# Kernel tuning notes

Measured on AMD Instinct MI355X. Metric: run time of the kernel, lower is better.

Reference implementation:

```python
import jax, jax.numpy as jnp
import numpy as np

SEQ, DM, STATE, BATCH = 1024, 512, 16, 8
D2 = 2 * DM
EPS = 1e-5


def rmsnorm(x, w):
    return x * jax.lax.rsqrt(jnp.mean(x * x, axis=-1, keepdims=True) + EPS) * w


def setup_inputs() -> dict:
    key = jax.random.key(0)
    ks = jax.random.split(key, 16)
    def lin(k, i, o):
        k1, k2 = jax.random.split(k)
        s = 1.0 / np.sqrt(i)
        return (jax.random.uniform(k1, (i, o), minval=-s, maxval=s),
                jax.random.uniform(k2, (o,), minval=-s, maxval=s))
    inp_w, inp_b = lin(ks[0], DM, D2)
    convlin_w, convlin_b = lin(ks[1], D2, D2)
    fc1_w, fc1_b = lin(ks[2], D2, D2)
    fc2_w, fc2_b = lin(ks[3], D2, STATE)
    fc3_w, fc3_b = lin(ks[4], D2, STATE)
    D_w, D_b = lin(ks[5], DM, D2)
    out_w, _ = lin(ks[6], D2, DM)
    out_b = jnp.ones((DM,))  # nn.init.constant_(out_proj.bias, 1.0)
    # Conv1d(seq_len, seq_len, k=3): weight (out_ch=SEQ, in_ch=SEQ, 3)
    s = 1.0 / np.sqrt(SEQ * 3)
    conv_w = jax.random.uniform(ks[7], (SEQ, SEQ, 3), minval=-s, maxval=s)
    conv_b = jax.random.uniform(ks[8], (SEQ,), minval=-s, maxval=s)
    norm_w = jnp.ones((DM,))
    x = jax.random.normal(ks[9], (BATCH, SEQ, DM))
    return dict(x=x, norm_w=norm_w, inp_w=inp_w, inp_b=inp_b, conv_w=conv_w,
                conv_b=conv_b, convlin_w=convlin_w, convlin_b=convlin_b,
                fc1_w=fc1_w, fc1_b=fc1_b, fc2_w=fc2_w, fc2_b=fc2_b,
                fc3_w=fc3_w, fc3_b=fc3_b, D_w=D_w, D_b=D_b,
                out_w=out_w, out_b=out_b)


def reference(x, norm_w, inp_w, inp_b, conv_w, conv_b, convlin_w, convlin_b,
              fc1_w, fc1_b, fc2_w, fc2_b, fc3_w, fc3_b, D_w, D_b, out_w, out_b):
    xn = rmsnorm(x, norm_w)                                  # (b, L, d)
    x_proj = xn @ inp_w + inp_b                              # (b, L, 2d)
    # Conv1d over channels=seq_len, spatial=2d, padding=1
    x_conv = jax.lax.conv_general_dilated(
        x_proj, conv_w, window_strides=(1,), padding=[(1, 1)],
        dimension_numbers=('NCH', 'OIH', 'NCH')) + conv_b[None, :, None]
    x_conv_out = jax.nn.silu(x_conv) @ convlin_w + convlin_b  # (b, L, 2d)
    # S6: h starts at zero so dA term vanishes; y = x*delta*sum_n(B*C)
    u = x_conv_out
    B = u @ fc2_w + fc2_b                                     # (b, L, n)
    C = u @ fc3_w + fc3_b                                     # (b, L, n)
    delta = jax.nn.softplus(u @ fc1_w + fc1_b)                # (b, L, 2d)
    bc = jnp.sum(B * C, axis=-1, keepdims=True)               # (b, L, 1)
    x_ssm = u * delta * bc                                    # (b, L, 2d)
    x_act = jax.nn.silu(x_ssm)
    x_residual = jax.nn.silu(xn @ D_w + D_b)
    return (x_residual * x_act) @ out_w + out_b               # (b, L, d)
```

## Files before the change

kernel.cpp:

```cpp
#include <hip/hip_runtime.h>
#include <hip/hip_bf16.h>

#define SEQ 1024
#define DM 512
#define D2 1024
#define NSTATE 16
#define BATCH 8
#define ROWS (BATCH * SEQ)
#define EPSF 1e-5f

typedef __attribute__((ext_vector_type(8))) short bf16x8;
typedef __attribute__((ext_vector_type(4))) float f32x4;

#define AS1 __attribute__((address_space(1)))
#define AS3 __attribute__((address_space(3)))

__device__ __forceinline__ void gll16(const void* g, void* l) {
    __builtin_amdgcn_global_load_lds(
        (const AS1 unsigned int*)(uintptr_t)g,
        (AS3 unsigned int*)(unsigned int)(uintptr_t)l, 16, 0, 0);
}

__device__ __forceinline__ float sigmoidf_(float x) {
    return 1.f / (1.f + __expf(-x));
}
__device__ __forceinline__ unsigned short f2bf(float f) {
    __hip_bfloat16 h = __float2bfloat16(f);
    unsigned short r;
    __builtin_memcpy(&r, &h, 2);
    return r;
}

__global__ __launch_bounds__(256) void tcvt_k(const float* __restrict__ src,
                                              __hip_bfloat16* __restrict__ dst,
                                              int R, int C) {
    __shared__ float tile[32][33];
    int c0 = blockIdx.x * 32, r0 = blockIdx.y * 32;
    int tx = threadIdx.x & 31, ty = threadIdx.x >> 5;
#pragma unroll
    for (int p = 0; p < 4; ++p) {
        int r = r0 + ty + p * 8, c = c0 + tx;
        if (r < R && c < C) tile[ty + p * 8][tx] = src[(size_t)r * C + c];
    }
    __syncthreads();
#pragma unroll
    for (int p = 0; p < 4; ++p) {
        int c = c0 + ty + p * 8, r = r0 + tx;
        if (r < R && c < C)
            dst[(size_t)c * R + r] = __float2bfloat16(tile[tx][ty + p * 8]);
    }
}

__global__ __launch_bounds__(256) void convw_k(const float* __restrict__ cw,
                                               __hip_bfloat16* __restrict__ wk) {
    int idx = blockIdx.x * 256 + threadIdx.x;
    float a = cw[(size_t)idx * 3 + 0];
    float b = cw[(size_t)idx * 3 + 1];
    float c = cw[(size_t)idx * 3 + 2];
    wk[idx] = __float2bfloat16(a);
    wk[(size_t)SEQ * SEQ + idx] = __float2bfloat16(b);
    wk[(size_t)2 * SEQ * SEQ + idx] = __float2bfloat16(c);
}

__global__ __launch_bounds__(256) void rmsnorm_k(
    const float* __restrict__ x, const float* __restrict__ w,
    __hip_bfloat16* __restrict__ o) {
    int row = blockIdx.x;
    const float* xr = x + (size_t)row * DM;
    __hip_bfloat16* orow = o + (size_t)row * DM;
    int t = threadIdx.x;
    float v0 = xr[t];
    float v1 = xr[t + 256];
    float ss = v0 * v0 + v1 * v1;
#pragma unroll
    for (int off = 32; off; off >>= 1) ss += __shfl_down(ss, off, 64);
    __shared__ float parts[4];
    if ((t & 63) == 0) parts[t >> 6] = ss;
    __syncthreads();
    float tot = parts[0] + parts[1] + parts[2] + parts[3];
    float rs = rsqrtf(tot * (1.f / DM) + EPSF);
    orow[t] = __float2bfloat16(v0 * rs * w[t]);
    orow[t + 256] = __float2bfloat16(v1 * rs * w[t + 256]);
}

template <int EPI>
__global__ __launch_bounds__(256) void mgemm(
    const __hip_bfloat16* __restrict__ A, const __hip_bfloat16* __restrict__ Bt,
    const float* __restrict__ bias, void* __restrict__ outp,
    void* __restrict__ outp2, const float* __restrict__ bias2,
    const __hip_bfloat16* __restrict__ uptr,
    const __hip_bfloat16* __restrict__ resid, const float* __restrict__ bcv,
    int M, int N, int K) {
    __shared__ __align__(16) __hip_bfloat16 As[3][128 * 32];
    __shared__ __align__(16) __hip_bfloat16 Bs[3][128 * 32];
    const int nbx = gridDim.x;
    int lin = blockIdx.y * nbx + blockIdx.x;
    int chunk = (nbx * gridDim.y) >> 3;
    int wg = (lin & 7) * chunk + (lin >> 3);
    const int n0 = (wg % nbx) * 128, m0 = (wg / nbx) * 128;
    const int t = threadIdx.x, lane = t & 63, w = t >> 6;
    const int wr = w >> 1, wc = w & 1;
    const int l15 = lane & 15, l4 = lane >> 4;

    const int r0_ = t >> 2, c0_ = (t & 3) ^ ((r0_ >> 1) & 3);
    const int b1 = 256 + t, r1_ = b1 >> 2, c1_ = (b1 & 3) ^ ((r1_ >> 1) & 3);
    const __hip_bfloat16* gA0 = A + (size_t)(m0 + r0_) * K + c0_ * 8;
    const __hip_bfloat16* gA1 = A + (size_t)(m0 + r1_) * K + c1_ * 8;
    const __hip_bfloat16* gB0 = Bt + (size_t)(n0 + r0_) * K + c0_ * 8;
    const __hip_bfloat16* gB1 = Bt + (size_t)(n0 + r1_) * K + c1_ * 8;
    const int d0 = (w * 64) * 8, d1 = (256 + w * 64) * 8;

    int offA[4], offB[4];
#pragma unroll
    for (int i = 0; i < 4; ++i) {
        int ra = wr * 64 + i * 16 + l15;
        offA[i] = (ra * 4 + (l4 ^ ((ra >> 1) & 3))) * 8;
        int rb = wc * 64 + i * 16 + l15;
        offB[i] = (rb * 4 + (l4 ^ ((rb >> 1) & 3))) * 8;
    }

#define MSTAGE(BUF, K0)                  \
    {                                    \
        gll16(gA0 + (K0), &As[BUF][d0]); \
        gll16(gA1 + (K0), &As[BUF][d1]); \
        gll16(gB0 + (K0), &Bs[BUF][d0]); \
        gll16(gB1 + (K0), &Bs[BUF][d1]); \
    }

    f32x4 acc[4][4] = {};
    const int NT = K >> 5;
    unsigned curb = 0, nxtb = 1, thdb = 2;
    MSTAGE(0, 0);
    MSTAGE(1, 32);
    asm volatile("s_waitcnt vmcnt(4)" ::: "memory");
    __builtin_amdgcn_s_barrier();
    __builtin_amdgcn_sched_barrier(0);

#pragma unroll 1
    for (int kt = 0; kt < NT; ++kt) {
        const bool st = (kt + 2 < NT);
        if (st) MSTAGE(thdb, (kt + 2) * 32);
        bf16x8 af[4], bv[4];
#pragma unroll
        for (int i = 0; i < 4; ++i) {
            af[i] = *(const bf16x8*)&As[curb][offA[i]];
            bv[i] = *(const bf16x8*)&Bs[curb][offB[i]];
        }
#pragma unroll
        for (int i = 0; i < 4; ++i)
#pragma unroll
            for (int j = 0; j < 4; ++j)
                acc[i][j] = __builtin_amdgcn_mfma_f32_16x16x32_bf16(
                    af[i], bv[j], acc[i][j], 0, 0, 0);
        if (kt + 1 < NT) {
            if (st)
                asm volatile("s_waitcnt vmcnt(4)" ::: "memory");
            else
                asm volatile("s_waitcnt vmcnt(0)" ::: "memory");
            __builtin_amdgcn_s_barrier();
            __builtin_amdgcn_sched_barrier(0);
        }
        unsigned tb = curb;
        curb = nxtb;
        nxtb = thdb;
        thdb = tb;
    }
#undef MSTAGE

    const int mb = m0 + wr * 64, nb = n0 + wc * 64;
#pragma unroll
    for (int i = 0; i < 4; ++i) {
#pragma unroll
        for (int j = 0; j < 4; ++j) {
            int ngl = nb + j * 16 + l15;
            if (EPI == 5) {
                if (nb < D2) {
                    float bj = bias[ngl];
                    int b = m0 >> 10;
                    int ibase = (mb & (SEQ - 1)) + i * 16 + l4 * 4;
                    ushort4 pk;
                    pk.x = f2bf(acc[i][j][0] + bj);
                    pk.y = f2bf(acc[i][j][1] + bj);
                    pk.z = f2bf(acc[i][j][2] + bj);
                    pk.w = f2bf(acc[i][j][3] + bj);
                    *(ushort4*)((__hip_bfloat16*)outp +
                                ((size_t)b * D2 + ngl) * SEQ + ibase) = pk;
                } else {
                    int ng2 = ngl - D2;
                    float bj = bias2[ng2];
#pragma unroll
                    for (int r = 0; r < 4; ++r) {
                        int mg = mb + i * 16 + l4 * 4 + r;
                        float c = acc[i][j][r] + bj;
                        ((__hip_bfloat16*)outp2)[(size_t)mg * D2 + ng2] =
                            __float2bfloat16(c * sigmoidf_(c));
                    }
                }
            } else {
                float bj = bias[ngl];
#pragma unroll
                for (int r = 0; r < 4; ++r) {
                    int mg = mb + i * 16 + l4 * 4 + r;
                    size_t ro = (size_t)mg * N + ngl;
                    float c = acc[i][j][r] + bj;
                    if (EPI == 1) {
                        ((__hip_bfloat16*)outp)[ro] = __float2bfloat16(c);
                    } else if (EPI == 3) {
                        float sp = (c > 20.f) ? c : log1pf(__expf(c));
                        float xs = __bfloat162float(uptr[ro]) * sp * bcv[mg];
                        float v = __bfloat162float(resid[ro]) *
                                  (xs * sigmoidf_(xs));
                        ((__hip_bfloat16*)outp)[ro] = __float2bfloat16(v);
                    } else {
                        ((float*)outp)[ro] = c;
                    }
                }
            }
        }
    }
}

__global__ __launch_bounds__(256) void conv_mfma(
    const __hip_bfloat16* __restrict__ wk,
    const __hip_bfloat16* __restrict__ Xt,
    const float* __restrict__ cb, __hip_bfloat16* __restrict__ outp) {
    __shared__ __align__(16) __hip_bfloat16 Ws[2][3][128 * 32];
    __shared__ __align__(16) __hip_bfloat16 Xs[2][128 * 32];
    __shared__ __align__(16) __hip_bfloat16 Xh[2][SEQ];
    int lin = blockIdx.x + 8 * blockIdx.y + 64 * blockIdx.z;
    int wg = (lin & 7) * 64 + (lin >> 3);
    const int n0 = (wg & 7) * 128;
    const int m0 = ((wg >> 3) & 7) * 128;
    const int z = wg >> 6;
    const int t = threadIdx.x, lane = t & 63, w = t >> 6;
    const int wr = w >> 1, wc = w & 1;
    const int l15 = lane & 15, l4 = lane >> 4;
    const __hip_bfloat16* Xtb = Xt + (size_t)z * D2 * SEQ;

    {
        int which = t >> 7;
        int col = (t & 127) * 8;
        int h = n0 - 1 + which * 129;
        uint4 v = make_uint4(0u, 0u, 0u, 0u);
        if (h >= 0 && h < D2)
            v = *(const uint4*)(Xtb + (size_t)h * SEQ + col);
        *(uint4*)&Xh[which][col] = v;
    }

    int rowp[2], cbw[2];
#pragma unroll
    for (int p = 0; p < 2; ++p) {
        int blk = p * 256 + t;
        rowp[p] = blk >> 2;
        cbw[p] = (blk & 3) ^ ((rowp[p] >> 1) & 3);
    }
    const __hip_bfloat16* wsrc[2][3];
    const __hip_bfloat16* xsrc[2];
#pragma unroll
    for (int p = 0; p < 2; ++p) {
#pragma unroll
        for (int tp = 0; tp < 3; ++tp)
            wsrc[p][tp] = wk + (size_t)tp * SEQ * SEQ +
                          (size_t)(m0 + rowp[p]) * SEQ + cbw[p] * 8;
        xsrc[p] = Xtb + (size_t)(n0 + rowp[p]) * SEQ + cbw[p] * 8;
    }
    const int dst0 = (w * 64) * 8, dst1 = (256 + w * 64) * 8;

    int offA[4];
#pragma unroll
    for (int i = 0; i < 4; ++i) {
        int ra = wr * 64 + i * 16 + l15;
        offA[i] = (ra * 4 + (l4 ^ ((ra >> 1) & 3))) * 8;
    }

#define CSTAGE(BUF, K0)                              \
    {                                                \
        gll16(wsrc[0][0] + (K0), &Ws[BUF][0][dst0]); \
        gll16(wsrc[1][0] + (K0), &Ws[BUF][0][dst1]); \
        gll16(wsrc[0][1] + (K0), &Ws[BUF][1][dst0]); \
        gll16(wsrc[1][1] + (K0), &Ws[BUF][1][dst1]); \
        gll16(wsrc[0][2] + (K0), &Ws[BUF][2][dst0]); \
        gll16(wsrc[1][2] + (K0), &Ws[BUF][2][dst1]); \
        gll16(xsrc[0] + (K0), &Xs[BUF][dst0]);       \
        gll16(xsrc[1] + (K0), &Xs[BUF][dst1]);       \
    }

    f32x4 acc[4][4] = {};
    CSTAGE(0, 0);
    asm volatile("s_waitcnt vmcnt(0) lgkmcnt(0)" ::: "memory");
    __builtin_amdgcn_s_barrier();
    __builtin_amdgcn_sched_barrier(0);

#pragma unroll 1
    for (int kt = 0; kt < 32; ++kt) {
        const int k0 = kt * 32;
        const int buf = kt & 1;
        if (kt + 1 < 32) CSTAGE(buf ^ 1, (kt + 1) * 32);
        bf16x8 aw[3][4];
#pragma unroll
        for (int tp = 0; tp < 3; ++tp)
#pragma unroll
            for (int i = 0; i < 4; ++i)
                aw[tp][i] = *(const bf16x8*)&Ws[buf][tp][offA[i]];
#pragma unroll
        for (int j = 0; j < 4; ++j) {
#pragma unroll
            for (int tp = 0; tp < 3; ++tp) {
                int rb = wc * 64 + j * 16 + l15 + tp;
                int r = rb - 1;
                const __hip_bfloat16* src =
                    &Xs[buf][(r * 4 + (l4 ^ ((r >> 1) & 3))) * 8];
                if (rb == 0) src = &Xh[0][k0 + l4 * 8];
                if (rb == 129) src = &Xh[1][k0 + l4 * 8];
                bf16x8 bvx = *(const bf16x8*)src;
#pragma unroll
                for (int i = 0; i < 4; ++i)
                    acc[i][j] = __builtin_amdgcn_mfma_f32_16x16x32_bf16(
                        aw[tp][i], bvx, acc[i][j], 0, 0, 0);
            }
        }
        if (kt + 1 < 32) {
            asm volatile("s_waitcnt vmcnt(0)" ::: "memory");
            __builtin_amdgcn_s_barrier();
            __builtin_amdgcn_sched_barrier(0);
        }
    }
#undef CSTAGE

    const int mb = m0 + wr * 64, nb = n0 + wc * 64;
    size_t ob = (size_t)z * SEQ * D2;
#pragma unroll
    for (int i = 0; i < 4; ++i)
#pragma unroll
        for (int j = 0; j < 4; ++j)
#pragma unroll
            for (int r = 0; r < 4; ++r) {
                int mg = mb + i * 16 + l4 * 4 + r;
                int ng = nb + j * 16 + l15;
                float c = acc[i][j][r] + cb[mg];
                outp[ob + (size_t)mg * D2 + ng] =
                    __float2bfloat16(c * sigmoidf_(c));
            }
}

__global__ __launch_bounds__(256) void bc2_k(
    const __hip_bfloat16* __restrict__ u, const __hip_bfloat16* __restrict__ fcT,
    const float* __restrict__ b2, const float* __restrict__ b3,
    float* __restrict__ bc) {
    __shared__ __align__(16) __hip_bfloat16 Bl[32 * 1024];
    __shared__ __align__(16) __hip_bfloat16 As[3][128 * 32];
    const int m0 = blockIdx.x * 128;
    const int t = threadIdx.x, lane = t & 63, w = t >> 6;
    const int l15 = lane & 15, l4 = lane >> 4;

#pragma unroll
    for (int it = 0; it < 16; ++it) {
        int q = it * 256 + t;
        int n = q >> 7, blk = q & 127;
        uint4 v = *(const uint4*)(fcT + (size_t)n * 1024 + blk * 8);
        *(uint4*)&Bl[(n * 128 + (blk ^ (n & 7))) * 8] = v;
    }

    const int r0_ = t >> 2, c0_ = (t & 3) ^ ((r0_ >> 1) & 3);
    const int bq = 256 + t, r1_ = bq >> 2, c1_ = (bq & 3) ^ ((r1_ >> 1) & 3);
    const __hip_bfloat16* gA0 = u + (size_t)(m0 + r0_) * 1024 + c0_ * 8;
    const __hip_bfloat16* gA1 = u + (size_t)(m0 + r1_) * 1024 + c1_ * 8;
    const int d0 = (w * 64) * 8, d1 = (256 + w * 64) * 8;

    int offA[2];
#pragma unroll
    for (int i = 0; i < 2; ++i) {
        int ra = w * 32 + i * 16 + l15;
        offA[i] = (ra * 4 + (l4 ^ ((ra >> 1) & 3))) * 8;
    }

#define BSTAGE(BUF, K0)                  \
    {                                    \
        gll16(gA0 + (K0), &As[BUF][d0]); \
        gll16(gA1 + (K0), &As[BUF][d1]); \
    }

    f32x4 acc[2][2] = {};
    unsigned curb = 0, nxtb = 1, thdb = 2;
    BSTAGE(0, 0);
    BSTAGE(1, 32);
    asm volatile("s_waitcnt vmcnt(2)" ::: "memory");
    __builtin_amdgcn_s_barrier();
    __builtin_amdgcn_sched_barrier(0);

#pragma unroll 1
    for (int kt = 0; kt < 32; ++kt) {
        const bool st = (kt + 2 < 32);
        if (st) BSTAGE(thdb, (kt + 2) * 32);
        bf16x8 af[2], bf[2];
#pragma unroll
        for (int i = 0; i < 2; ++i) af[i] = *(const bf16x8*)&As[curb][offA[i]];
#pragma unroll
        for (int nj = 0; nj < 2; ++nj) {
            int n = nj * 16 + l15;
            int blk = (kt * 4 + l4) ^ (n & 7);
            bf[nj] = *(const bf16x8*)&Bl[(n * 128 + blk) * 8];
        }
#pragma unroll
        for (int i = 0; i < 2; ++i)
#pragma unroll
            for (int nj = 0; nj < 2; ++nj)
                acc[i][nj] = __builtin_amdgcn_mfma_f32_16x16x32_bf16(
                    af[i], bf[nj], acc[i][nj], 0, 0, 0);
        if (kt + 1 < 32) {
            if (st)
                asm volatile("s_waitcnt vmcnt(2)" ::: "memory");
            else
                asm volatile("s_waitcnt vmcnt(0)" ::: "memory");
            __builtin_amdgcn_s_barrier();
            __builtin_amdgcn_sched_barrier(0);
        }
        unsigned tb = curb;
        curb = nxtb;
        nxtb = thdb;
        thdb = tb;
    }
#undef BSTAGE

    float bb2 = b2[l15], bb3 = b3[l15];
#pragma unroll
    for (int i = 0; i < 2; ++i)
#pragma unroll
        for (int r = 0; r < 4; ++r) {
            float Bv = acc[i][0][r] + bb2;
            float Cv = acc[i][1][r] + bb3;
            float p = Bv * Cv;
            p += __shfl_xor(p, 1, 64);
            p += __shfl_xor(p, 2, 64);
            p += __shfl_xor(p, 4, 64);
            p += __shfl_xor(p, 8, 64);
            if (l15 == 0)
                bc[m0 + w * 32 + i * 16 + l4 * 4 + r] = p;
        }
}

extern "C" void kernel_launch(void* const* d_in, const int* in_sizes, int n_in,
                              void* d_out, int out_size, void* d_ws,
                              size_t ws_size, hipStream_t stream) {
    const float* x = (const float*)d_in[0];
    const float* norm_w = (const float*)d_in[1];
    const float* inp_w = (const float*)d_in[2];
    const float* inp_b = (const float*)d_in[3];
    const float* conv_w = (const float*)d_in[4];
    const float* conv_b = (const float*)d_in[5];
    const float* convlin_w = (const float*)d_in[6];
    const float* convlin_b = (const float*)d_in[7];
    const float* fc1_w = (const float*)d_in[8];
    const float* fc1_b = (const float*)d_in[9];
    const float* fc2_w = (const float*)d_in[10];
    const float* fc2_b = (const float*)d_in[11];
    const float* fc3_w = (const float*)d_in[12];
    const float* fc3_b = (const float*)d_in[13];
    const float* D_w = (const float*)d_in[14];
    const float* D_b = (const float*)d_in[15];
    const float* out_w = (const float*)d_in[16];
    const float* out_b = (const float*)d_in[17];
    float* out = (float*)d_out;

    __hip_bfloat16* xnb = (__hip_bfloat16*)d_ws;
    __hip_bfloat16* xt = xnb + (size_t)ROWS * DM;
    __hip_bfloat16* cvo = xt + (size_t)BATCH * D2 * SEQ;
    __hip_bfloat16* u = cvo + (size_t)ROWS * D2;
    __hip_bfloat16* resid = u + (size_t)ROWS * D2;
    __hip_bfloat16* Wcat = resid + (size_t)ROWS * D2;
    __hip_bfloat16* clT = Wcat + (size_t)2 * D2 * DM;
    __hip_bfloat16* fc1T = clT + (size_t)D2 * D2;
    __hip_bfloat16* outT = fc1T + (size_t)D2 * D2;
    __hip_bfloat16* wk = outT + (size_t)DM * D2;
    __hip_bfloat16* fcT = wk + (size_t)3 * SEQ * SEQ;
    float* bcb = (float*)(fcT + (size_t)32 * D2);

    tcvt_k<<<dim3(D2 / 32, DM / 32), 256, 0, stream>>>(inp_w, Wcat, DM, D2);
    tcvt_k<<<dim3(D2 / 32, DM / 32), 256, 0, stream>>>(
        D_w, Wcat + (size_t)D2 * DM, DM, D2);
    tcvt_k<<<dim3(D2 / 32, D2 / 32), 256, 0, stream>>>(convlin_w, clT, D2, D2);
    tcvt_k<<<dim3(D2 / 32, D2 / 32), 256, 0, stream>>>(fc1_w, fc1T, D2, D2);
    tcvt_k<<<dim3(DM / 32, D2 / 32), 256, 0, stream>>>(out_w, outT, D2, DM);
    tcvt_k<<<dim3(1, D2 / 32), 256, 0, stream>>>(fc2_w, fcT, D2, NSTATE);
    tcvt_k<<<dim3(1, D2 / 32), 256, 0, stream>>>(fc3_w, fcT + (size_t)16 * D2,
                                                 D2, NSTATE);
    convw_k<<<SEQ * SEQ / 256, 256, 0, stream>>>(conv_w, wk);
    rmsnorm_k<<<ROWS, 256, 0, stream>>>(x, norm_w, xnb);
    mgemm<5><<<dim3(2 * D2 / 128, ROWS / 128), 256, 0, stream>>>(
        xnb, Wcat, inp_b, xt, resid, D_b, nullptr, nullptr, nullptr, ROWS,
        2 * D2, DM);
    conv_mfma<<<dim3(D2 / 128, SEQ / 128, BATCH), 256, 0, stream>>>(
        wk, xt, conv_b, cvo);
    mgemm<1><<<dim3(D2 / 128, ROWS / 128), 256, 0, stream>>>(
        cvo, clT, convlin_b, u, nullptr, nullptr, nullptr, nullptr, nullptr,
        ROWS, D2, D2);
    bc2_k<<<ROWS / 128, 256, 0, stream>>>(u, fcT, fc2_b, fc3_b, bcb);
    mgemm<3><<<dim3(D2 / 128, ROWS / 128), 256, 0, stream>>>(
        u, fc1T, fc1_b, cvo, nullptr, nullptr, u, resid, bcb, ROWS, D2, D2);
    mgemm<4><<<dim3(DM / 128, ROWS / 128), 256, 0, stream>>>(
        cvo, outT, out_b, out, nullptr, nullptr, nullptr, nullptr, nullptr,
        ROWS, DM, D2);
}
```

Measured before the change: 241.9 us.

## Merge weight-transpose launches, add MFMA priority hints, restructure conv pipeline waits

Seven separate transpose-and-convert launches become one kernel that selects its matrix from blockIdx.z, so fewer launches and their gaps remain. s_setprio is raised around the MFMA blocks in both the GEMM and the conv kernels to favour the wave issuing matrix instructions. The conv kernel's double-buffer loop now waits with vmcnt(8) after issuing the next stage, instead of a full vmcnt(0) at the end of each iteration, which lets the prefetch overlap compute. The merged launch spawns many early-exit blocks for the small matrices, and the new wait counts depend on exact per-thread load ordering.

```diff
diff --git a/kernel.cpp b/kernel.cpp
--- a/kernel.cpp
+++ b/kernel.cpp
@@ -31,11 +31,28 @@
     return r;
 }
 
-__global__ __launch_bounds__(256) void tcvt_k(const float* __restrict__ src,
-                                              __hip_bfloat16* __restrict__ dst,
-                                              int R, int C) {
+__global__ __launch_bounds__(256) void prep_all(
+    const float* s0, const float* s1, const float* s2, const float* s3,
+    const float* s4, const float* s5, const float* s6,
+    __hip_bfloat16* d0, __hip_bfloat16* d1, __hip_bfloat16* d2,
+    __hip_bfloat16* d3, __hip_bfloat16* d4, __hip_bfloat16* d5,
+    __hip_bfloat16* d6) {
+    const int j = blockIdx.z;
+    int R, C;
+    const float* src;
+    __hip_bfloat16* dst;
+    switch (j) {
+        case 0: src = s0; dst = d0; R = 512; C = 1024; break;
+        case 1: src = s1; dst = d1; R = 512; C = 1024; break;
+        case 2: src = s2; dst = d2; R = 1024; C = 1024; break;
+        case 3: src = s3; dst = d3; R = 1024; C = 1024; break;
+        case 4: src = s4; dst = d4; R = 1024; C = 512; break;
+        case 5: src = s5; dst = d5; R = 1024; C = 16; break;
+        default: src = s6; dst = d6; R = 1024; C = 16; break;
+    }
+    int c0 = blockIdx.x * 32, r0 = blockIdx.y * 32;
+    if (c0 >= C || r0 >= R) return;
     __shared__ float tile[32][33];
-    int c0 = blockIdx.x * 32, r0 = blockIdx.y * 32;
     int tx = threadIdx.x & 31, ty = threadIdx.x >> 5;
 #pragma unroll
     for (int p = 0; p < 4; ++p) {
@@ -146,12 +163,14 @@
             af[i] = *(const bf16x8*)&As[curb][offA[i]];
             bv[i] = *(const bf16x8*)&Bs[curb][offB[i]];
         }
+        __builtin_amdgcn_s_setprio(1);
 #pragma unroll
         for (int i = 0; i < 4; ++i)
 #pragma unroll
             for (int j = 0; j < 4; ++j)
                 acc[i][j] = __builtin_amdgcn_mfma_f32_16x16x32_bf16(
                     af[i], bv[j], acc[i][j], 0, 0, 0);
+        __builtin_amdgcn_s_setprio(0);
         if (kt + 1 < NT) {
             if (st)
                 asm volatile("s_waitcnt vmcnt(4)" ::: "memory");
@@ -287,21 +306,27 @@
 
     f32x4 acc[4][4] = {};
     CSTAGE(0, 0);
-    asm volatile("s_waitcnt vmcnt(0) lgkmcnt(0)" ::: "memory");
-    __builtin_amdgcn_s_barrier();
-    __builtin_amdgcn_sched_barrier(0);
+    asm volatile("s_waitcnt lgkmcnt(0)" ::: "memory");
 
 #pragma unroll 1
     for (int kt = 0; kt < 32; ++kt) {
         const int k0 = kt * 32;
         const int buf = kt & 1;
-        if (kt + 1 < 32) CSTAGE(buf ^ 1, (kt + 1) * 32);
+        if (kt + 1 < 32) {
+            CSTAGE(buf ^ 1, (kt + 1) * 32);
+            asm volatile("s_waitcnt vmcnt(8)" ::: "memory");
+        } else {
+            asm volatile("s_waitcnt vmcnt(0)" ::: "memory");
+        }
+        __builtin_amdgcn_s_barrier();
+        __builtin_amdgcn_sched_barrier(0);
         bf16x8 aw[3][4];
 #pragma unroll
         for (int tp = 0; tp < 3; ++tp)
 #pragma unroll
             for (int i = 0; i < 4; ++i)
                 aw[tp][i] = *(const bf16x8*)&Ws[buf][tp][offA[i]];
+        __builtin_amdgcn_s_setprio(1);
 #pragma unroll
         for (int j = 0; j < 4; ++j) {
 #pragma unroll
@@ -319,8 +344,8 @@
                         aw[tp][i], bvx, acc[i][j], 0, 0, 0);
             }
         }
+        __builtin_amdgcn_s_setprio(0);
         if (kt + 1 < 32) {
-            asm volatile("s_waitcnt vmcnt(0)" ::: "memory");
             __builtin_amdgcn_s_barrier();
             __builtin_amdgcn_sched_barrier(0);
         }
@@ -475,15 +500,9 @@
     __hip_bfloat16* fcT = wk + (size_t)3 * SEQ * SEQ;
     float* bcb = (float*)(fcT + (size_t)32 * D2);
 
-    tcvt_k<<<dim3(D2 / 32, DM / 32), 256, 0, stream>>>(inp_w, Wcat, DM, D2);
-    tcvt_k<<<dim3(D2 / 32, DM / 32), 256, 0, stream>>>(
-        D_w, Wcat + (size_t)D2 * DM, DM, D2);
-    tcvt_k<<<dim3(D2 / 32, D2 / 32), 256, 0, stream>>>(convlin_w, clT, D2, D2);
-    tcvt_k<<<dim3(D2 / 32, D2 / 32), 256, 0, stream>>>(fc1_w, fc1T, D2, D2);
-    tcvt_k<<<dim3(DM / 32, D2 / 32), 256, 0, stream>>>(out_w, outT, D2, DM);
-    tcvt_k<<<dim3(1, D2 / 32), 256, 0, stream>>>(fc2_w, fcT, D2, NSTATE);
-    tcvt_k<<<dim3(1, D2 / 32), 256, 0, stream>>>(fc3_w, fcT + (size_t)16 * D2,
-                                                 D2, NSTATE);
+    prep_all<<<dim3(32, 32, 7), 256, 0, stream>>>(
+        inp_w, D_w, convlin_w, fc1_w, out_w, fc2_w, fc3_w, Wcat,
+        Wcat + (size_t)D2 * DM, clT, fc1T, outT, fcT, fcT + (size_t)16 * D2);
     convw_k<<<SEQ * SEQ / 256, 256, 0, stream>>>(conv_w, wk);
     rmsnorm_k<<<ROWS, 256, 0, stream>>>(x, norm_w, xnb);
     mgemm<5><<<dim3(2 * D2 / 128, ROWS / 128), 256, 0, stream>>>(
```

After: 225.0 us. 1.08x faster.
